# Kernel tuning notes

Measured on AMD Instinct MI355X. Metric: run time of the kernel, lower is better.

The kernel has to match this reference:

```python
import jax, jax.numpy as jnp
import numpy as np

N_AGENTS = 8
STATE_DIM = 256
NODE = 2 * N_AGENTS          # 16 graph nodes per sample
FEAT = STATE_DIM // NODE     # 16
NHID = 4
NHEADS = 4
GOUT = 2 * FEAT              # 32 = gat_output
EMBED = 32                   # mixing_embed_dim
ALPHA = 0.2                  # leaky relu slope in GAT
LAYER_IN = NODE * GOUT       # 512 = state_dim * 2
BS = 2048
T = 128


def setup_inputs() -> dict:
    key = jax.random.key(0)
    ks = jax.random.split(key, 16)
    r = lambda i, shape: jax.random.normal(ks[i], shape, dtype=jnp.float32) * 0.1
    return dict(
        agent_qs=jax.random.normal(ks[0], (BS, T, N_AGENTS), dtype=jnp.float32),
        states=jax.random.normal(ks[1], (BS, T, STATE_DIM), dtype=jnp.float32),
        # GAT params: 4 attention heads + output attention layer
        W_heads=r(2, (NHEADS, FEAT, NHID)),
        a_heads=r(3, (NHEADS, 2 * NHID, 1)),
        W_out=r(4, (NHEADS * NHID, GOUT)),
        a_out=r(5, (2 * GOUT, 1)),
        # hypernet params (torch Linear stored as [in, out])
        hw1_w=r(6, (LAYER_IN, EMBED * N_AGENTS)), hw1_b=r(7, (EMBED * N_AGENTS,)),
        hb1_w=r(8, (LAYER_IN, EMBED)), hb1_b=r(9, (EMBED,)),
        hwf_w=r(10, (LAYER_IN, EMBED)), hwf_b=r(11, (EMBED,)),
        v1_w=r(12, (LAYER_IN, EMBED)), v1_b=r(13, (EMBED,)),
        v2_w=r(14, (EMBED, 1)), v2_b=r(15, (1,)),
    )


def _gat_layer(x, W, a, concat):
    # Standard pyGAT GraphAttentionLayer; adj is all-ones so no masking needed.
    Wh = x @ W                       # [N, F']
    Fo = W.shape[1]
    e1 = Wh @ a[:Fo]                 # [N, 1]
    e2 = Wh @ a[Fo:]                 # [N, 1]
    e = jax.nn.leaky_relu(e1 + e2.T, ALPHA)  # [N, N]
    att = jax.nn.softmax(e, axis=1)
    h = att @ Wh                     # [N, F']
    return jax.nn.elu(h) if concat else h


def _gat(x, W_heads, a_heads, W_out, a_out):
    # x: [NODE, FEAT] -> [NODE, GOUT]; dropout is identity (eval mode)
    heads = jax.vmap(lambda W, a: _gat_layer(x, W, a, True))(W_heads, a_heads)  # [H, N, NHID]
    h = jnp.transpose(heads, (1, 0, 2)).reshape(x.shape[0], NHEADS * NHID)      # concat heads
    return jax.nn.elu(_gat_layer(h, W_out, a_out, False))


def reference(agent_qs, states, W_heads, a_heads, W_out, a_out,
              hw1_w, hw1_b, hb1_w, hb1_b, hwf_w, hwf_b,
              v1_w, v1_b, v2_w, v2_b):
    bs, t = agent_qs.shape[0], agent_qs.shape[1]
    nodes = states.reshape(bs * t, NODE, FEAT)
    # batched GAT over all (batch*time) tiny graphs (replaces Python loops)
    gat = jax.vmap(lambda x: _gat(x, W_heads, a_heads, W_out, a_out))(nodes)  # [bt, N, GOUT]
    s = gat.reshape(bs * t, LAYER_IN)
    qs = agent_qs.reshape(bs * t, 1, N_AGENTS)
    # QMIX mixing with hypernetworks
    w1 = jnp.abs(s @ hw1_w + hw1_b).reshape(-1, N_AGENTS, EMBED)
    b1 = (s @ hb1_w + hb1_b).reshape(-1, 1, EMBED)
    hidden = jax.nn.elu(jnp.einsum('bij,bjk->bik', qs, w1) + b1)  # [bt, 1, EMBED]
    w_final = jnp.abs(s @ hwf_w + hwf_b).reshape(-1, EMBED, 1)
    v = (jax.nn.relu(s @ v1_w + v1_b) @ v2_w + v2_b).reshape(-1, 1, 1)
    y = jnp.einsum('bij,bjk->bik', hidden, w_final) + v          # [bt, 1, 1]
    return y.reshape(bs, t, 1)
```

## Files before the change

kernel.cpp:

```cpp
#include <hip/hip_runtime.h>
#include <hip/hip_bf16.h>
#include <stdint.h>


#define BT       (2048 * 128)
#define ALPHA    0.2f
#define LOG2E    1.4426950408889634f
#define NTIL32   11
#define AUXOFF   360448

typedef __attribute__((ext_vector_type(8))) short bf16x8;
typedef __attribute__((ext_vector_type(16))) float f32x16;
typedef __attribute__((ext_vector_type(2))) float f32x2;
typedef _Float16 f16x2 __attribute__((ext_vector_type(2)));

__device__ __forceinline__ f32x2 b2(float s) { return (f32x2){s, s}; }
__device__ __forceinline__ f32x2 pkfma(f32x2 a, f32x2 b, f32x2 c) {
    return __builtin_elementwise_fma(a, b, c);
}
__device__ __forceinline__ float elu1(float x) { return x > 0.f ? x : (__expf(x) - 1.f); }

__device__ __forceinline__ float fexp2(float x) {
#if __has_builtin(__builtin_amdgcn_exp2f)
    return __builtin_amdgcn_exp2f(x);
#else
    return exp2f(x);
#endif
}

__device__ __forceinline__ unsigned short f32_to_bf16_rne(float x) {
    uint32_t u = __float_as_uint(x);
    u += 0x7fffu + ((u >> 16) & 1u);
    return (unsigned short)(u >> 16);
}

__device__ __forceinline__ float fdot2f(uint32_t a, f16x2 b, float c) {
#if __has_builtin(__builtin_amdgcn_fdot2)
    return __builtin_amdgcn_fdot2(__builtin_bit_cast(f16x2, a), b, c, false);
#else
    const f16x2 av = __builtin_bit_cast(f16x2, a);
    return fmaf((float)av.x, (float)b.x, fmaf((float)av.y, (float)b.y, c));
#endif
}
__device__ __forceinline__ f16x2 pkrtz(float a, float b) {
    return __builtin_bit_cast(f16x2, __builtin_amdgcn_cvt_pkrtz(a, b));
}
__device__ __forceinline__ uint32_t cvtpk_bf16(float lo, float hi) {
    uint32_t r;
    asm("v_cvt_pk_bf16_f32 %0, %1, %2" : "=v"(r) : "v"(lo), "v"(hi));
    return r;
}
__device__ __forceinline__ float bf_lo(uint32_t u) { return __uint_as_float(u << 16); }
__device__ __forceinline__ float bf_hi(uint32_t u) { return __uint_as_float(u & 0xffff0000u); }
__device__ __forceinline__ f32x16 z16() {
    f32x16 r;
    #pragma unroll
    for (int i = 0; i < 16; ++i) r[i] = 0.f;
    return r;
}

__device__ __forceinline__ f32x2 softmax16x(const float* e2A, const float* e2B,
                                            f32x2 e1, f32x2* ee) {
    #pragma unroll
    for (int t4 = 0; t4 < 4; ++t4) {
        const float4 va = *(const float4*)&e2A[t4 * 4];
        const float4 vb = *(const float4*)&e2B[t4 * 4];
        const f32x2 l0 = e1 + (f32x2){va.x, vb.x};
        const f32x2 l1 = e1 + (f32x2){va.y, vb.y};
        const f32x2 l2 = e1 + (f32x2){va.z, vb.z};
        const f32x2 l3 = e1 + (f32x2){va.w, vb.w};
        const f32x2 k0 = __builtin_elementwise_max(l0, l0 * b2(ALPHA));
        const f32x2 k1 = __builtin_elementwise_max(l1, l1 * b2(ALPHA));
        const f32x2 k2 = __builtin_elementwise_max(l2, l2 * b2(ALPHA));
        const f32x2 k3 = __builtin_elementwise_max(l3, l3 * b2(ALPHA));
        ee[4*t4+0] = (f32x2){fexp2(k0.x), fexp2(k0.y)};
        ee[4*t4+1] = (f32x2){fexp2(k1.x), fexp2(k1.y)};
        ee[4*t4+2] = (f32x2){fexp2(k2.x), fexp2(k2.y)};
        ee[4*t4+3] = (f32x2){fexp2(k3.x), fexp2(k3.y)};
    }
    f32x2 s0 = ee[0]+ee[1], s1 = ee[2]+ee[3], s2 = ee[4]+ee[5], s3 = ee[6]+ee[7];
    f32x2 s4 = ee[8]+ee[9], s5 = ee[10]+ee[11], s6 = ee[12]+ee[13], s7 = ee[14]+ee[15];
    s0 += s1; s2 += s3; s4 += s5; s6 += s7;
    const f32x2 sum = (s0 + s2) + (s4 + s6);
    return (f32x2){__builtin_amdgcn_rcpf(sum.x), __builtin_amdgcn_rcpf(sum.y)};
}

__global__ __launch_bounds__(256) void pack_b(
    const float* __restrict__ hw1_w, const float* __restrict__ hb1_w,
    const float* __restrict__ hwf_w, const float* __restrict__ v1_w,
    const float* __restrict__ W_out, const float* __restrict__ a_out,
    unsigned short* __restrict__ bpack, float* __restrict__ aux)
{
    const int gi = blockIdx.x * 256 + threadIdx.x;
    if (gi < 32 * NTIL32 * 64) {
        const int l   = gi & 63;
        const int ti  = (gi >> 6) % NTIL32;
        const int kt2 = gi / (NTIL32 * 64);
        const int col = ti * 32 + (l & 31);
        const int k0  = kt2 * 16 + (l >> 5) * 8;
        const float* src; int stride; int c;
        if (col < 256)      { src = hw1_w; stride = 256; c = col; }
        else if (col < 288) { src = hb1_w; stride = 32;  c = col - 256; }
        else if (col < 320) { src = hwf_w; stride = 32;  c = col - 288; }
        else                { src = v1_w;  stride = 32;  c = col - 320; }
        union { unsigned short u[8]; uint4 v; } pk;
        #pragma unroll
        for (int e = 0; e < 8; ++e) {
            const int k = k0 + e;
            const int r_old = ((k & 15) << 5) + (k >> 4);
            pk.u[e] = f32_to_bf16_rne(src[(long)r_old * stride + c]);
        }
        ((uint4*)bpack)[gi] = pk.v;
    } else if (gi < 32 * NTIL32 * 64 + 32) {
        const int a = gi - 32 * NTIL32 * 64;
        const int which = a >> 4, f = a & 15;
        float s = 0.f;
        for (int c = 0; c < 32; ++c) s = fmaf(W_out[f * 32 + c], a_out[which * 32 + c], s);
        aux[a] = s * LOG2E;
    }
}

__global__ __launch_bounds__(256) void fused_kernel(
    const float* __restrict__ agent_qs, const float* __restrict__ states,
    const float* __restrict__ W_heads,  const float* __restrict__ a_heads,
    const float* __restrict__ W_out,    const float* __restrict__ a_out,
    const unsigned short* __restrict__ bpack, const float* __restrict__ aux,
    const float* __restrict__ hw1_b, const float* __restrict__ hb1_b,
    const float* __restrict__ hwf_b, const float* __restrict__ v1_b,
    const float* __restrict__ v2_w,  const float* __restrict__ v2_b,
    float* __restrict__ out)
{
    __shared__ unsigned short A[32][512];
    float* bst  = (float*)((char*)&A[0][0] + 25344);
    float* qs   = (float*)((char*)&A[0][0] + 26880);
    float* cont = (float*)((char*)&A[0][0] + 28032);

    const int t    = threadIdx.x;
    const int w    = t >> 6;
    const int lane = t & 63;
    const int g    = lane >> 4;
    const int n    = lane & 15;
    const long sbase = (long)blockIdx.x * 32;

    char* scr = (char*)&A[0][0] + w * 8192;
    _Float16* hxA = (_Float16*)(scr + (g * 2)     * 528);
    _Float16* hxB = (_Float16*)(scr + (g * 2 + 1) * 528);
    float*    e2A = (float*)(scr + 4224 + (g * 2)     * 272);
    float*    e2B = (float*)(scr + 4224 + (g * 2 + 1) * 272);

    const int mA = w * 8 + g;
    const int mB = w * 8 + 4 + g;

    const float bv0 = hw1_b[t];
    float bv1 = 0.f;
    if (t < 32)       bv1 = hb1_b[t];
    else if (t < 64)  bv1 = hwf_b[t - 32];
    else if (t < 96)  bv1 = v1_b[t - 64];
    else if (t < 128) bv1 = v2_w[t - 96];
    const float qv = agent_qs[sbase * 8 + t];

    f32x2 xr2[16];
    {
        const float4* xa = (const float4*)(states + (sbase + mA) * 256 + n * 16);
        const float4* xb = (const float4*)(states + (sbase + mB) * 256 + n * 16);
        #pragma unroll
        for (int i = 0; i < 4; ++i) {
            const float4 va = xa[i], vb = xb[i];
            xr2[4*i+0] = (f32x2){va.x, vb.x};
            xr2[4*i+1] = (f32x2){va.y, vb.y};
            xr2[4*i+2] = (f32x2){va.z, vb.z};
            xr2[4*i+3] = (f32x2){va.w, vb.w};
        }
    }

    f32x2 e1s[4];
    #pragma unroll
    for (int h = 0; h < 4; ++h) {
        f32x2 wh0 = b2(0.f), wh1 = b2(0.f), wh2 = b2(0.f), wh3 = b2(0.f);
        #pragma unroll
        for (int f = 0; f < 16; ++f) {
            const f32x2 xf = xr2[f];
            wh0 = pkfma(xf, b2(W_heads[h*64 + f*4 + 0]), wh0);
            wh1 = pkfma(xf, b2(W_heads[h*64 + f*4 + 1]), wh1);
            wh2 = pkfma(xf, b2(W_heads[h*64 + f*4 + 2]), wh2);
            wh3 = pkfma(xf, b2(W_heads[h*64 + f*4 + 3]), wh3);
        }
        const f32x2 e1 = pkfma(wh0, b2(a_heads[h*8+0]),
                         pkfma(wh1, b2(a_heads[h*8+1]),
                         pkfma(wh2, b2(a_heads[h*8+2]), wh3 * b2(a_heads[h*8+3]))));
        const f32x2 e2 = pkfma(wh0, b2(a_heads[h*8+4]),
                         pkfma(wh1, b2(a_heads[h*8+5]),
                         pkfma(wh2, b2(a_heads[h*8+6]), wh3 * b2(a_heads[h*8+7]))));
        e1s[h] = e1 * b2(LOG2E);
        const f32x2 e2L = e2 * b2(LOG2E);
        hxA[h*64 + 0*16 + n] = (_Float16)wh0.x;  hxB[h*64 + 0*16 + n] = (_Float16)wh0.y;
        hxA[h*64 + 1*16 + n] = (_Float16)wh1.x;  hxB[h*64 + 1*16 + n] = (_Float16)wh1.y;
        hxA[h*64 + 2*16 + n] = (_Float16)wh2.x;  hxB[h*64 + 2*16 + n] = (_Float16)wh2.y;
        hxA[h*64 + 3*16 + n] = (_Float16)wh3.x;  hxB[h*64 + 3*16 + n] = (_Float16)wh3.y;
        e2A[h*16 + n] = e2L.x;
        e2B[h*16 + n] = e2L.y;
    }

    f32x2 hcat2[16];
    #pragma unroll
    for (int h = 0; h < 4; ++h) {
        f32x2 ee[16];
        const f32x2 inv = softmax16x(e2A + h*16, e2B + h*16, e1s[h], ee);
        f16x2 eA[8], eB[8];
        #pragma unroll
        for (int jp = 0; jp < 8; ++jp) {
            eA[jp] = pkrtz(ee[2*jp].x, ee[2*jp+1].x);
            eB[jp] = pkrtz(ee[2*jp].y, ee[2*jp+1].y);
        }
        #pragma unroll
        for (int k = 0; k < 4; ++k) {
            const uint4 wa0 = *(const uint4*)&hxA[h*64 + k*16];
            const uint4 wa1 = *(const uint4*)&hxA[h*64 + k*16 + 8];
            const uint4 wb0 = *(const uint4*)&hxB[h*64 + k*16];
            const uint4 wb1 = *(const uint4*)&hxB[h*64 + k*16 + 8];
            float sA = 0.f, sB = 0.f;
            sA = fdot2f(wa0.x, eA[0], sA);  sB = fdot2f(wb0.x, eB[0], sB);
            sA = fdot2f(wa0.y, eA[1], sA);  sB = fdot2f(wb0.y, eB[1], sB);
            sA = fdot2f(wa0.z, eA[2], sA);  sB = fdot2f(wb0.z, eB[2], sB);
            sA = fdot2f(wa0.w, eA[3], sA);  sB = fdot2f(wb0.w, eB[3], sB);
            sA = fdot2f(wa1.x, eA[4], sA);  sB = fdot2f(wb1.x, eB[4], sB);
            sA = fdot2f(wa1.y, eA[5], sA);  sB = fdot2f(wb1.y, eB[5], sB);
            sA = fdot2f(wa1.z, eA[6], sA);  sB = fdot2f(wb1.z, eB[6], sB);
            sA = fdot2f(wa1.w, eA[7], sA);  sB = fdot2f(wb1.w, eB[7], sB);
            hcat2[h*4+k] = (f32x2){elu1(sA * inv.x), elu1(sB * inv.y)};
        }
    }

    f32x2 e1o = b2(0.f), e2o = b2(0.f);
    #pragma unroll
    for (int f = 0; f < 16; ++f) {
        e1o = pkfma(hcat2[f], b2(aux[f]), e1o);
        e2o = pkfma(hcat2[f], b2(aux[16 + f]), e2o);
    }
    e2A[n] = e2o.x;
    e2B[n] = e2o.y;
    f32x2 ee[16];
    const f32x2 invo = softmax16x(e2A, e2B, e1o, ee);
    #pragma unroll
    for (int j = 0; j < 16; ++j) ee[j] *= invo;

    {
        uint32_t hA[8], hB[8], aAv[8], aBv[8];
        #pragma unroll
        for (int p2 = 0; p2 < 8; ++p2) {
            hA[p2]  = cvtpk_bf16(hcat2[2*p2].x, hcat2[2*p2+1].x);
            hB[p2]  = cvtpk_bf16(hcat2[2*p2].y, hcat2[2*p2+1].y);
            aAv[p2] = cvtpk_bf16(ee[2*p2].x, ee[2*p2+1].x);
            aBv[p2] = cvtpk_bf16(ee[2*p2].y, ee[2*p2+1].y);
        }
        char* hb = scr + g * 1024;
        char* ab = scr + (4 + g) * 1024;
        uint4 v;
        v.x=hA[0]; v.y=hA[1]; v.z=hA[2]; v.w=hA[3];  *(uint4*)(hb + n*32)       = v;
        v.x=hA[4]; v.y=hA[5]; v.z=hA[6]; v.w=hA[7];  *(uint4*)(hb + n*32 + 16)  = v;
        v.x=hB[0]; v.y=hB[1]; v.z=hB[2]; v.w=hB[3];  *(uint4*)(hb + 512 + n*32) = v;
        v.x=hB[4]; v.y=hB[5]; v.z=hB[6]; v.w=hB[7];  *(uint4*)(hb + 512 + n*32 + 16) = v;
        v.x=aAv[0];v.y=aAv[1];v.z=aAv[2];v.w=aAv[3]; *(uint4*)(ab + n*32)       = v;
        v.x=aAv[4];v.y=aAv[5];v.z=aAv[6];v.w=aAv[7]; *(uint4*)(ab + n*32 + 16)  = v;
        v.x=aBv[0];v.y=aBv[1];v.z=aBv[2];v.w=aBv[3]; *(uint4*)(ab + 512 + n*32) = v;
        v.x=aBv[4];v.y=aBv[5];v.z=aBv[6];v.w=aBv[7]; *(uint4*)(ab + 512 + n*32 + 16) = v;
    }

    const int row  = lane & 31;
    const int half = lane >> 5;
    bf16x8 wf;
    {
        union { uint32_t d[4]; bf16x8 v; } u;
        #pragma unroll
        for (int e = 0; e < 4; ++e)
            u.d[e] = cvtpk_bf16(W_out[(half*8 + 2*e)*32 + row],
                                W_out[(half*8 + 2*e + 1)*32 + row]);
        wf = u.v;
    }

    #pragma unroll 1
    for (int gg = 0; gg < 4; ++gg) {
        const char* hb = scr + gg * 1024;
        const char* ab = scr + (4 + gg) * 1024;
        uint4 af1u = *(const uint4*)(hb + (row & 15) * 32 + (row >> 4) * 512 + half * 16);
        bf16x8 af1; memcpy(&af1, &af1u, 16);
        f32x16 D1 = __builtin_amdgcn_mfma_f32_32x32x16_bf16(af1, wf, z16(), 0, 0, 0);

        const uint32_t d0 = cvtpk_bf16(D1[0], D1[1]),   d1 = cvtpk_bf16(D1[2], D1[3]);
        const uint32_t d2 = cvtpk_bf16(D1[4], D1[5]),   d3 = cvtpk_bf16(D1[6], D1[7]);
        const uint32_t f0 = cvtpk_bf16(D1[8], D1[9]),   f1 = cvtpk_bf16(D1[10], D1[11]);
        const uint32_t f2 = cvtpk_bf16(D1[12], D1[13]), f3 = cvtpk_bf16(D1[14], D1[15]);
        const uint32_t x0 = (uint32_t)__shfl_xor((int)d0, 32);
        const uint32_t x1 = (uint32_t)__shfl_xor((int)d1, 32);
        const uint32_t x2 = (uint32_t)__shfl_xor((int)d2, 32);
        const uint32_t x3 = (uint32_t)__shfl_xor((int)d3, 32);
        const uint32_t y0 = (uint32_t)__shfl_xor((int)f0, 32);
        const uint32_t y1 = (uint32_t)__shfl_xor((int)f1, 32);
        const uint32_t y2 = (uint32_t)__shfl_xor((int)f2, 32);
        const uint32_t y3 = (uint32_t)__shfl_xor((int)f3, 32);
        union { uint32_t d[4]; bf16x8 v; } b1u, b2u;
        if (half == 0) {
            b1u.d[0]=d0; b1u.d[1]=d1; b1u.d[2]=x0; b1u.d[3]=x1;
            b2u.d[0]=f0; b2u.d[1]=f1; b2u.d[2]=y0; b2u.d[3]=y1;
        } else {
            b1u.d[0]=x2; b1u.d[1]=x3; b1u.d[2]=d2; b1u.d[3]=d3;
            b2u.d[0]=y2; b2u.d[1]=y3; b2u.d[2]=f2; b2u.d[3]=f3;
        }

        uint4 aau = {0,0,0,0}, abu = {0,0,0,0};
        if (row < 16) aau = *(const uint4*)(ab + row * 32 + half * 16);
        else          abu = *(const uint4*)(ab + 512 + (row - 16) * 32 + half * 16);
        bf16x8 aaf, abf; memcpy(&aaf, &aau, 16); memcpy(&abf, &abu, 16);
        f32x16 D2 = __builtin_amdgcn_mfma_f32_32x32x16_bf16(aaf, b1u.v, z16(), 0, 0, 0);
        D2 = __builtin_amdgcn_mfma_f32_32x32x16_bf16(abf, b2u.v, D2, 0, 0, 0);

        const int c = row;
        const int mAg = w * 8 + gg, mBg = w * 8 + 4 + gg;
        const uint32_t pA0 = cvtpk_bf16(elu1(D2[0]),  elu1(D2[1]));
        const uint32_t pA1 = cvtpk_bf16(elu1(D2[2]),  elu1(D2[3]));
        const uint32_t pA2 = cvtpk_bf16(elu1(D2[4]),  elu1(D2[5]));
        const uint32_t pA3 = cvtpk_bf16(elu1(D2[6]),  elu1(D2[7]));
        const uint32_t pB0 = cvtpk_bf16(elu1(D2[8]),  elu1(D2[9]));
        const uint32_t pB1 = cvtpk_bf16(elu1(D2[10]), elu1(D2[11]));
        const uint32_t pB2 = cvtpk_bf16(elu1(D2[12]), elu1(D2[13]));
        const uint32_t pB3 = cvtpk_bf16(elu1(D2[14]), elu1(D2[15]));
        const int u0 = 2 * c, u1 = 2 * c + 1;
        const int pa0 = (((u0 & 3) << 4) + (u0 >> 2) + mAg) & 63;
        const int pa1 = (((u1 & 3) << 4) + (u1 >> 2) + mAg) & 63;
        const int pb0 = (((u0 & 3) << 4) + (u0 >> 2) + mBg) & 63;
        const int pb1 = (((u1 & 3) << 4) + (u1 >> 2) + mBg) & 63;
        uint2 wv;
        wv.x = pA0; wv.y = pA1;
        *(uint2*)((char*)&A[0][0] + mAg * 1024 + pa0 * 16 + half * 8) = wv;
        wv.x = pA2; wv.y = pA3;
        *(uint2*)((char*)&A[0][0] + mAg * 1024 + pa1 * 16 + half * 8) = wv;
        wv.x = pB0; wv.y = pB1;
        *(uint2*)((char*)&A[0][0] + mBg * 1024 + pb0 * 16 + half * 8) = wv;
        wv.x = pB2; wv.y = pB3;
        *(uint2*)((char*)&A[0][0] + mBg * 1024 + pb1 * 16 + half * 8) = wv;
    }

    __syncthreads();

    const int ti0 = w * 3;
    f32x16 acc0 = z16(), acc1 = z16(), acc2v = z16();

    for (int kt2 = 0; kt2 < 32; ++kt2) {
        const int u = 2 * kt2 + half;
        const int phys = (((u & 3) << 4) + (u >> 2) + row) & 63;
        uint4 au = *(const uint4*)((const char*)&A[0][0] + row * 1024 + phys * 16);
        bf16x8 af; memcpy(&af, &au, 16);
        const uint4* bp = (const uint4*)bpack + (kt2 * NTIL32 + ti0) * 64 + lane;
        uint4 bw0 = bp[0];
        uint4 bw1 = bp[64];
        bf16x8 bf0, bf1;
        memcpy(&bf0, &bw0, 16); memcpy(&bf1, &bw1, 16);
        acc0 = __builtin_amdgcn_mfma_f32_32x32x16_bf16(af, bf0, acc0, 0, 0, 0);
        acc1 = __builtin_amdgcn_mfma_f32_32x32x16_bf16(af, bf1, acc1, 0, 0, 0);
        if (w < 3) {
            uint4 bw2 = bp[128];
            bf16x8 bf2; memcpy(&bf2, &bw2, 16);
            acc2v = __builtin_amdgcn_mfma_f32_32x32x16_bf16(af, bf2, acc2v, 0, 0, 0);
        }
    }

    __syncthreads();

    {
        f32x16 av[3] = {acc0, acc1, acc2v};
        const int ntj = (w < 3) ? 3 : 2;
        #pragma unroll
        for (int j = 0; j < 3; ++j) {
            if (j >= ntj) break;
            const int e = (ti0 + j) * 32 + row;
            char* hp = (char*)&A[0][0] + e * 72;
            #pragma unroll
            for (int grp = 0; grp < 4; ++grp) {
                const int m0 = grp * 8 + 4 * half;
                uint2 v;
                v.x = cvtpk_bf16(av[j][grp*4+0], av[j][grp*4+1]);
                v.y = cvtpk_bf16(av[j][grp*4+2], av[j][grp*4+3]);
                *(uint2*)(hp + m0 * 2) = v;
            }
        }
    }
    bst[t] = bv0;
    if (t < 128) bst[256 + t] = bv1;
    qs[(t >> 3) * 9 + (t & 7)] = qv;
    __syncthreads();

    #pragma unroll
    for (int it = 0; it < 2; ++it) {
        const int slot = t + it * 256;
        const int mp   = slot >> 5;
        const int emb  = slot & 31;
        const int m0   = mp * 2;
        const char* base = (const char*)&A[0][0] + m0 * 2;
        const uint32_t ub1 = *(const uint32_t*)(base + (256 + emb) * 72);
        const float bb1 = bst[256 + emb];
        float h0 = bf_lo(ub1) + bb1;
        float h1 = bf_hi(ub1) + bb1;
        #pragma unroll
        for (int a = 0; a < 8; ++a) {
            const uint32_t uw = *(const uint32_t*)(base + (a * 32 + emb) * 72);
            const float bw_ = bst[a * 32 + emb];
            h0 = fmaf(qs[m0 * 9 + a],       fabsf(bf_lo(uw) + bw_), h0);
            h1 = fmaf(qs[(m0 + 1) * 9 + a], fabsf(bf_hi(uw) + bw_), h1);
        }
        const uint32_t uwf = *(const uint32_t*)(base + (288 + emb) * 72);
        const uint32_t uv1 = *(const uint32_t*)(base + (320 + emb) * 72);
        const float bwf = bst[288 + emb], bv1e = bst[320 + emb], v2we = bst[352 + emb];
        cont[m0 * 32 + emb]       = elu1(h0) * fabsf(bf_lo(uwf) + bwf)
                                  + fmaxf(bf_lo(uv1) + bv1e, 0.f) * v2we;
        cont[(m0 + 1) * 32 + emb] = elu1(h1) * fabsf(bf_hi(uwf) + bwf)
                                  + fmaxf(bf_hi(uv1) + bv1e, 0.f) * v2we;
    }
    __syncthreads();

    if (t < 32) {
        float y = 0.f;
        #pragma unroll
        for (int e = 0; e < 32; ++e) y += cont[t * 32 + ((t + e) & 31)];
        out[sbase + t] = y + v2_b[0];
    }
}

extern "C" void kernel_launch(void* const* d_in, const int* in_sizes, int n_in,
                              void* d_out, int out_size, void* d_ws, size_t ws_size,
                              hipStream_t stream) {
    const float* agent_qs = (const float*)d_in[0];
    const float* states   = (const float*)d_in[1];
    const float* W_heads  = (const float*)d_in[2];
    const float* a_heads  = (const float*)d_in[3];
    const float* W_out    = (const float*)d_in[4];
    const float* a_out    = (const float*)d_in[5];
    const float* hw1_w    = (const float*)d_in[6];
    const float* hw1_b    = (const float*)d_in[7];
    const float* hb1_w    = (const float*)d_in[8];
    const float* hb1_b    = (const float*)d_in[9];
    const float* hwf_w    = (const float*)d_in[10];
    const float* hwf_b    = (const float*)d_in[11];
    const float* v1_w     = (const float*)d_in[12];
    const float* v1_b     = (const float*)d_in[13];
    const float* v2_w     = (const float*)d_in[14];
    const float* v2_b     = (const float*)d_in[15];

    unsigned short* bpack = (unsigned short*)d_ws;
    float* aux = (float*)((char*)d_ws + AUXOFF);

    pack_b<<<(32 * NTIL32 * 64 + 32 + 255) / 256, 256, 0, stream>>>(
        hw1_w, hb1_w, hwf_w, v1_w, W_out, a_out, bpack, aux);
    fused_kernel<<<BT / 32, 256, 0, stream>>>(agent_qs, states,
                                              W_heads, a_heads, W_out, a_out,
                                              bpack, aux,
                                              hw1_b, hb1_b, hwf_b, v1_b, v2_w, v2_b,
                                              (float*)d_out);
}
```

Before: 286.9 us.

## Software-pipeline B global loads and A LDS loads in the MFMA k-loop

Restructures the hypernet GEMM k-loop so the packed B weight fragments are prefetched from global memory two iterations ahead, and the A fragment is loaded from LDS one iteration ahead, in rotating registers. MFMA issue is wrapped in s_setprio raises so this wave's matrix ops get priority over other waves. The aim is to hide global/LDS latency behind the matrix instructions. The cost is extra register pressure, which may lower occupancy, and the loop is forced not to unroll.

New measurement: 328.9 us. 1.15x slower.

```diff
diff --git a/kernel.cpp b/kernel.cpp
--- a/kernel.cpp
+++ b/kernel.cpp
@@ -345,23 +345,44 @@
     const int ti0 = w * 3;
     f32x16 acc0 = z16(), acc1 = z16(), acc2v = z16();
 
-    for (int kt2 = 0; kt2 < 32; ++kt2) {
+    const uint4* bbase = (const uint4*)bpack + ti0 * 64 + lane;
+    uint4 p0a = bbase[0],            p0b = bbase[64];
+    uint4 p1a = bbase[NTIL32 * 64],  p1b = bbase[NTIL32 * 64 + 64];
+    uint4 p0c = {0,0,0,0}, p1c = {0,0,0,0};
+    if (w < 3) { p0c = bbase[128]; p1c = bbase[NTIL32 * 64 + 128]; }
+
+    auto lda = [&](int kt2) -> uint4 {
         const int u = 2 * kt2 + half;
         const int phys = (((u & 3) << 4) + (u >> 2) + row) & 63;
-        uint4 au = *(const uint4*)((const char*)&A[0][0] + row * 1024 + phys * 16);
-        bf16x8 af; memcpy(&af, &au, 16);
-        const uint4* bp = (const uint4*)bpack + (kt2 * NTIL32 + ti0) * 64 + lane;
-        uint4 bw0 = bp[0];
-        uint4 bw1 = bp[64];
-        bf16x8 bf0, bf1;
-        memcpy(&bf0, &bw0, 16); memcpy(&bf1, &bw1, 16);
+        return *(const uint4*)((const char*)&A[0][0] + row * 1024 + phys * 16);
+    };
+    uint4 acur = lda(0);
+
+    #pragma unroll 1
+    for (int kt2 = 0; kt2 < 32; ++kt2) {
+        const uint4 ca = p0a, cb = p0b, cc = p0c;
+        p0a = p1a; p0b = p1b; p0c = p1c;
+        if (kt2 < 30) {
+            const uint4* bn = bbase + (kt2 + 2) * (NTIL32 * 64);
+            p1a = bn[0]; p1b = bn[64];
+            if (w < 3) p1c = bn[128];
+        }
+        uint4 anxt = acur;
+        if (kt2 < 31) anxt = lda(kt2 + 1);
+
+        bf16x8 af, bf0, bf1;
+        memcpy(&af, &acur, 16);
+        memcpy(&bf0, &ca, 16);
+        memcpy(&bf1, &cb, 16);
+        __builtin_amdgcn_s_setprio(1);
         acc0 = __builtin_amdgcn_mfma_f32_32x32x16_bf16(af, bf0, acc0, 0, 0, 0);
         acc1 = __builtin_amdgcn_mfma_f32_32x32x16_bf16(af, bf1, acc1, 0, 0, 0);
         if (w < 3) {
-            uint4 bw2 = bp[128];
-            bf16x8 bf2; memcpy(&bf2, &bw2, 16);
+            bf16x8 bf2; memcpy(&bf2, &cc, 16);
             acc2v = __builtin_amdgcn_mfma_f32_32x32x16_bf16(af, bf2, acc2v, 0, 0, 0);
         }
+        __builtin_amdgcn_s_setprio(0);
+        acur = anxt;
     }
 
     __syncthreads();
```
